# Optimization experiments

Measured on AMD Instinct MI355X. Metric: run time of the kernel, lower is better.

The kernel has to match this reference:

```python
import jax, jax.numpy as jnp
import numpy as np

VOCAB, EMB, HID, LABELS, NUM_LAYERS = 32000, 512, 1024, 64, 2
B, S = 32, 512


def setup_inputs() -> dict:
    key = jax.random.key(0)
    ks = jax.random.split(key, 12)
    s_e = 1.0 / np.sqrt(EMB)
    s_h = 1.0 / np.sqrt(HID)
    inp = {
        "tokens": jax.random.randint(ks[0], (B, S), 0, VOCAB),
        "emb": jax.random.normal(ks[1], (VOCAB, EMB), jnp.float32),
        # layer 0: input dim EMB
        "W_ih0": jax.random.uniform(ks[2], (HID, EMB), jnp.float32, -s_h, s_h),
        "W_hh0": jax.random.uniform(ks[3], (HID, HID), jnp.float32, -s_h, s_h),
        "b_ih0": jax.random.uniform(ks[4], (HID,), jnp.float32, -s_h, s_h),
        "b_hh0": jax.random.uniform(ks[5], (HID,), jnp.float32, -s_h, s_h),
        # layer 1: input dim HID
        "W_ih1": jax.random.uniform(ks[6], (HID, HID), jnp.float32, -s_h, s_h),
        "W_hh1": jax.random.uniform(ks[7], (HID, HID), jnp.float32, -s_h, s_h),
        "b_ih1": jax.random.uniform(ks[8], (HID,), jnp.float32, -s_h, s_h),
        "b_hh1": jax.random.uniform(ks[9], (HID,), jnp.float32, -s_h, s_h),
        "W_out": jax.random.uniform(ks[10], (LABELS, HID), jnp.float32, -s_h, s_h),
        "b_out": jax.random.uniform(ks[11], (LABELS,), jnp.float32, -s_h, s_h),
    }
    return inp


def _rnn_layer(x, W_ih, W_hh, b_ih, b_hh):
    # x: [B,S,in] -> h_t = tanh(W_ih x_t + b_ih + W_hh h_{t-1} + b_hh)
    # Precompute input projection for all timesteps (one big GEMM).
    xp = jnp.einsum('bsi,hi->bsh', x, W_ih) + (b_ih + b_hh)  # [B,S,H]
    h0 = jnp.zeros((x.shape[0], W_hh.shape[0]), x.dtype)

    def step(h, xt):
        h = jnp.tanh(xt + h @ W_hh.T)
        return h, h

    _, ys = jax.lax.scan(step, h0, jnp.swapaxes(xp, 0, 1))  # [S,B,H]
    return jnp.swapaxes(ys, 0, 1)  # [B,S,H]


def reference(tokens, emb, W_ih0, W_hh0, b_ih0, b_hh0,
              W_ih1, W_hh1, b_ih1, b_hh1, W_out, b_out):
    x = emb[tokens]  # [B,S,EMB]
    h = _rnn_layer(x, W_ih0, W_hh0, b_ih0, b_hh0)
    h = _rnn_layer(h, W_ih1, W_hh1, b_ih1, b_hh1)
    return jnp.einsum('bsh,lh->bsl', h, W_out) + b_out  # [B,S,LABELS]
```

## Files before the change

### kernel.cpp

```cpp
#include <hip/hip_runtime.h>
#include <math.h>

#define B_    32
#define S_    512
#define EMB_  512
#define HID_  1024
#define LAB_  64
#define M_    (B_ * S_)

#define SLOT_U64   2048
#define LS_STRIDE  (8 * SLOT_U64)
#define EX_TOTAL   (2 * 4 * LS_STRIDE)
#define EPBIT      0x40000000u
#define NANPAT64   0x7FC000007FC00000ULL
#define ONEPAT64   0x3F8000003F800000ULL
#define PAYMASK    0xBFFFFFFFu

typedef unsigned int u32x4 __attribute__((ext_vector_type(4)));

__device__ __forceinline__ void astore64(unsigned long long* p, unsigned long long v) {
    __hip_atomic_store(p, v, __ATOMIC_RELAXED, __HIP_MEMORY_SCOPE_AGENT);
}
__device__ __forceinline__ void apoll2(const unsigned long long* q0,
                                       const unsigned long long* q1,
                                       u32x4& w0, u32x4& w1) {
    asm volatile(
        "global_load_dwordx4 %0, %2, off sc1\n\t"
        "global_load_dwordx4 %1, %3, off sc1\n\t"
        "s_waitcnt vmcnt(0)"
        : "=&v"(w0), "=&v"(w1)
        : "v"(q0), "v"(q1)
        : "memory");
}
__device__ __forceinline__ bool epok4(u32x4 v, unsigned eb) {
    return ((((v[0] ^ eb) | (v[1] ^ eb)) | ((v[2] ^ eb) | (v[3] ^ eb)))
            & EPBIT) == 0;
}
__device__ __forceinline__ float fold16(float* v, int kg) {
#pragma unroll
    for (int st = 0; st < 4; ++st) {
        const int m  = 1 << st;
        const int nh = 8 >> st;
        const bool hi = (kg & m) != 0;
#pragma unroll
        for (int j = 0; j < 8; ++j) {
            if (j < nh) {
                const float a0 = v[2*j], a1 = v[2*j+1];
                const float got = __shfl_xor(hi ? a0 : a1, m, 64);
                v[j] = (hi ? a1 : a0) + got;
            }
        }
    }
    float r = v[0];
    r += __shfl_xor(r, 16, 64);
    r += __shfl_xor(r, 32, 64);
    return r;
}

__global__ __launch_bounds__(256) void gemm_bias(
    const float* __restrict__ A, const int* __restrict__ tokens,
    const float* __restrict__ W, const float* __restrict__ bias,
    const float* __restrict__ bias2, float* __restrict__ C,
    int M, int K, int N)
{
    __shared__ float As[128][17];
    __shared__ float Ws[64][17];

    const int tid = threadIdx.x;
    const int tx  = tid & 15;
    const int ty  = tid >> 4;
    const int n0  = blockIdx.x * 64;
    const int m0  = blockIdx.y * 128;

    const int lr  = tid >> 2;
    const int lk  = (tid & 3) << 2;

    const int ar0 = tokens ? tokens[m0 + lr]      : (m0 + lr);
    const int ar1 = tokens ? tokens[m0 + 64 + lr] : (m0 + 64 + lr);
    const float* __restrict__ arow0 = A + (size_t)ar0 * K;
    const float* __restrict__ arow1 = A + (size_t)ar1 * K;
    const float* __restrict__ wrow  = W + (size_t)(n0 + lr) * K;

    float bs[4];
#pragma unroll
    for (int j = 0; j < 4; ++j) {
        int n = n0 + tx * 4 + j;
        bs[j] = bias[n] + (bias2 ? bias2[n] : 0.0f);
    }

    float acc[8][4] = {};

    for (int k0 = 0; k0 < K; k0 += 16) {
        const float4 a0 = *(const float4*)(arow0 + k0 + lk);
        const float4 a1 = *(const float4*)(arow1 + k0 + lk);
        const float4 wv = *(const float4*)(wrow  + k0 + lk);
        __syncthreads();
        As[lr][lk + 0] = a0.x; As[lr][lk + 1] = a0.y;
        As[lr][lk + 2] = a0.z; As[lr][lk + 3] = a0.w;
        As[64 + lr][lk + 0] = a1.x; As[64 + lr][lk + 1] = a1.y;
        As[64 + lr][lk + 2] = a1.z; As[64 + lr][lk + 3] = a1.w;
        Ws[lr][lk + 0] = wv.x; Ws[lr][lk + 1] = wv.y;
        Ws[lr][lk + 2] = wv.z; Ws[lr][lk + 3] = wv.w;
        __syncthreads();

#pragma unroll
        for (int kk = 0; kk < 16; ++kk) {
            float b[4], a[8];
#pragma unroll
            for (int j = 0; j < 4; ++j) b[j] = Ws[tx * 4 + j][kk];
#pragma unroll
            for (int i = 0; i < 8; ++i) a[i] = As[ty * 8 + i][kk];
#pragma unroll
            for (int i = 0; i < 8; ++i)
#pragma unroll
                for (int j = 0; j < 4; ++j)
                    acc[i][j] += a[i] * b[j];
        }
    }

#pragma unroll
    for (int i = 0; i < 8; ++i) {
        const int m = m0 + ty * 8 + i;
        float4 v;
        v.x = acc[i][0] + bs[0];
        v.y = acc[i][1] + bs[1];
        v.z = acc[i][2] + bs[2];
        v.w = acc[i][3] + bs[3];
        *(float4*)(C + (size_t)m * N + n0 + tx * 4) = v;
    }
}

__global__ __launch_bounds__(256) void fill_poison(unsigned long long* p, int n)
{
    const int i = blockIdx.x * 256 + threadIdx.x;
    if (i < n) {
        const int ls = i / LS_STRIDE;
        p[i] = (ls == 4) ? ONEPAT64 : NANPAT64;
    }
}

__global__ __launch_bounds__(512, 2) void rnn_fused(
    const float* __restrict__ Whh0, const float* __restrict__ Whh1,
    const float* __restrict__ Wih1, const float* __restrict__ b_ih1,
    const float* __restrict__ b_hh1, float* __restrict__ xb,
    unsigned long long* __restrict__ ex)
{
    extern __shared__ float smem[];
    float2* hb = (float2*)smem;

    const int wg  = blockIdx.x;
    const int g   = wg & 7;
    const int s   = wg >> 3;
    const int tid = threadIdx.x;
    const int j8  = tid >> 6;
    const int kg  = tid & 63;
    const int b0  = g * 4;

    float w0[4][16], wx[4][16], wh[4][16];
    {
        const size_t base = (size_t)(s * 32 + j8 * 4) * HID_ + kg;
#pragma unroll
        for (int i = 0; i < 4; ++i)
#pragma unroll
            for (int q = 0; q < 16; ++q) {
                const size_t o = base + (size_t)i * HID_ + (size_t)q * 64;
                w0[i][q] = Whh0[o];
                wx[i][q] = Wih1[o];
                wh[i][q] = Whh1[o];
            }
    }

    const int i4 = (kg >> 2) & 3;
    const int bb = kg & 3;
    const int ok = s * 32 + j8 * 4 + i4;
    float bsum = 0.f;
    if (kg < 16) bsum = b_ih1[ok] + b_hh1[ok];

    float* px0 = xb + ((size_t)(b0 + bb) * S_) * HID_ + ok;
    float* px1 = px0;

    unsigned long long* const exg = ex + (size_t)g * SLOT_U64;
    const int c0 = 2 * tid, c1 = 1024 + 2 * tid;

    for (int r = 0; r <= S_; ++r) {
        float xpv = 0.f;
        if (kg < 16 && r < S_) xpv = *px0;
        px0 += HID_;

        const int cur = r & 1;
        float2* s0 = hb + (size_t)cur * 2048;
        float2* s1 = hb + (size_t)(2 + cur) * 2048;

        const int sl = (r - 1) & 3;
        const unsigned eb = ((((unsigned)(r - 1)) >> 2) & 1u) << 30;

        if (r == 0) {
#pragma unroll
            for (int k = 0; k < 4; ++k)
                s0[tid + 512 * k] = make_float2(0.f, 0.f);
        } else {
            const unsigned long long* pl = exg + (size_t)sl * LS_STRIDE;
            unsigned pend = 3u;
            u32x4 w0v, w1v;
            do {
                apoll2(pl + c0, pl + c1, w0v, w1v);
                if ((pend & 1u) && epok4(w0v, eb)) {
                    s0[tid]        = make_float2(
                        __uint_as_float(w0v[0] & PAYMASK),
                        __uint_as_float(w0v[1] & PAYMASK));
                    s0[1024 + tid] = make_float2(
                        __uint_as_float(w0v[2] & PAYMASK),
                        __uint_as_float(w0v[3] & PAYMASK));
                    pend &= ~1u;
                }
                if ((pend & 2u) && epok4(w1v, eb)) {
                    s0[512 + tid]  = make_float2(
                        __uint_as_float(w1v[0] & PAYMASK),
                        __uint_as_float(w1v[1] & PAYMASK));
                    s0[1536 + tid] = make_float2(
                        __uint_as_float(w1v[2] & PAYMASK),
                        __uint_as_float(w1v[3] & PAYMASK));
                    pend &= ~2u;
                }
            } while (pend);
        }
        __syncthreads();

        {
            float v[16] = {};
#pragma unroll
            for (int q = 0; q < 16; ++q) {
                const float2 a0 = s0[q * 64 + kg];
                const float2 a1 = s0[1024 + q * 64 + kg];
#pragma unroll
                for (int i = 0; i < 4; ++i) {
                    const float fa = w0[i][q];
                    v[i*4+0] += fa * a0.x; v[i*4+1] += fa * a0.y;
                    v[i*4+2] += fa * a1.x; v[i*4+3] += fa * a1.y;
                }
            }
            const float r0 = fold16(v, kg);
            if (r < S_) {
                float h0 = 0.f;
                if (kg < 16) h0 = tanhf(xpv + r0);
                const float h0p = __shfl_xor(h0, 1, 64);
                if (kg < 16 && (bb & 1) == 0) {
                    const unsigned pe = (((unsigned)r >> 2) & 1u) << 30;
                    const unsigned long long u =
                        ((unsigned long long)(__float_as_uint(h0p) | pe) << 32) |
                        (unsigned long long)(__float_as_uint(h0) | pe);
                    astore64(exg + (size_t)(r & 3) * LS_STRIDE
                                 + 2 * ok + (bb >> 1), u);
                }
            }
        }

        if (r == 1) {
#pragma unroll
            for (int k = 0; k < 4; ++k)
                s1[tid + 512 * k] = make_float2(0.f, 0.f);
        } else if (r >= 2) {
            const unsigned long long* pl = exg + (size_t)(4 + sl) * LS_STRIDE;
            unsigned pend = 3u;
            u32x4 w0v, w1v;
            do {
                apoll2(pl + c0, pl + c1, w0v, w1v);
                if ((pend & 1u) && epok4(w0v, eb)) {
                    s1[tid]        = make_float2(
                        __uint_as_float(w0v[0] & PAYMASK),
                        __uint_as_float(w0v[1] & PAYMASK));
                    s1[1024 + tid] = make_float2(
                        __uint_as_float(w0v[2] & PAYMASK),
                        __uint_as_float(w0v[3] & PAYMASK));
                    pend &= ~1u;
                }
                if ((pend & 2u) && epok4(w1v, eb)) {
                    s1[512 + tid]  = make_float2(
                        __uint_as_float(w1v[0] & PAYMASK),
                        __uint_as_float(w1v[1] & PAYMASK));
                    s1[1536 + tid] = make_float2(
                        __uint_as_float(w1v[2] & PAYMASK),
                        __uint_as_float(w1v[3] & PAYMASK));
                    pend &= ~2u;
                }
            } while (pend);
        }
        __syncthreads();

        if (r >= 1) {
            float v[16] = {};
#pragma unroll
            for (int q = 0; q < 16; ++q) {
                const float2 a0 = s0[q * 64 + kg];
                const float2 a1 = s0[1024 + q * 64 + kg];
                const float2 c0f = s1[q * 64 + kg];
                const float2 c1f = s1[1024 + q * 64 + kg];
#pragma unroll
                for (int i = 0; i < 4; ++i) {
                    const float fb = wx[i][q];
                    v[i*4+0] += fb * a0.x; v[i*4+1] += fb * a0.y;
                    v[i*4+2] += fb * a1.x; v[i*4+3] += fb * a1.y;
                    const float fc = wh[i][q];
                    v[i*4+0] += fc * c0f.x; v[i*4+1] += fc * c0f.y;
                    v[i*4+2] += fc * c1f.x; v[i*4+3] += fc * c1f.y;
                }
            }
            const float r1 = fold16(v, kg);
            float h1 = 0.f;
            if (kg < 16) h1 = tanhf(r1 + bsum);
            const float h1p = __shfl_xor(h1, 1, 64);
            if (kg < 16) *px1 = h1;
            if (kg < 16 && (bb & 1) == 0) {
                const unsigned pe = (((unsigned)r >> 2) & 1u) << 30;
                const unsigned long long u =
                    ((unsigned long long)(__float_as_uint(h1p) | pe) << 32) |
                    (unsigned long long)(__float_as_uint(h1) | pe);
                astore64(exg + (size_t)(4 + (r & 3)) * LS_STRIDE
                             + 2 * ok + (bb >> 1), u);
            }
            px1 += HID_;
        }
    }
}

extern "C" void kernel_launch(void* const* d_in, const int* in_sizes, int n_in,
                              void* d_out, int out_size, void* d_ws, size_t ws_size,
                              hipStream_t stream)
{
    const int*   tokens = (const int*)  d_in[0];
    const float* emb    = (const float*)d_in[1];
    const float* W_ih0  = (const float*)d_in[2];
    const float* W_hh0  = (const float*)d_in[3];
    const float* b_ih0  = (const float*)d_in[4];
    const float* b_hh0  = (const float*)d_in[5];
    const float* W_ih1  = (const float*)d_in[6];
    const float* W_hh1  = (const float*)d_in[7];
    const float* b_ih1  = (const float*)d_in[8];
    const float* b_hh1  = (const float*)d_in[9];
    const float* W_out  = (const float*)d_in[10];
    const float* b_out  = (const float*)d_in[11];
    float* out = (float*)d_out;

    float* buf = (float*)d_ws;
    unsigned long long* ex = (unsigned long long*)d_out;

    const size_t scan_lds = 98304;
    hipFuncSetAttribute((const void*)rnn_fused,
                        hipFuncAttributeMaxDynamicSharedMemorySize, (int)scan_lds);

    gemm_bias<<<dim3(HID_ / 64, M_ / 128), 256, 0, stream>>>(
        emb, tokens, W_ih0, b_ih0, b_hh0, buf, M_, EMB_, HID_);

    fill_poison<<<EX_TOTAL / 256, 256, 0, stream>>>(ex, EX_TOTAL);

    rnn_fused<<<256, 512, scan_lds, stream>>>(
        W_hh0, W_hh1, W_ih1, b_ih1, b_hh1, buf, ex);

    gemm_bias<<<dim3(LAB_ / 64, M_ / 128), 256, 0, stream>>>(
        buf, nullptr, W_out, b_out, nullptr, out, M_, HID_, LAB_);
}
```

Measured before the change: 3.258 ms.

## Skew layer-1 recurrence by two steps and merge both polls into one barrier

Layer 1 now runs two steps behind layer 0 and reads layer-0 state from a triple-buffered shared slot. Both exchange polls (layer-0 h at r-1 and layer-1 h at r-3) therefore happen in a single combined wait loop with one __syncthreads per step instead of two. This removes a serialized global poll and barrier from each timestep's critical path, letting the cross-workgroup latencies of the two layers overlap. It costs one extra loop iteration, more LDS buffers, and more complex epoch and slot indexing, which could cause hangs or wrong results if any index is off.

```diff
diff --git a/kernel.cpp b/kernel.cpp
--- a/kernel.cpp
+++ b/kernel.cpp
@@ -13,7 +13,6 @@
 #define EX_TOTAL   (2 * 4 * LS_STRIDE)
 #define EPBIT      0x40000000u
 #define NANPAT64   0x7FC000007FC00000ULL
-#define ONEPAT64   0x3F8000003F800000ULL
 #define PAYMASK    0xBFFFFFFFu
 
 typedef unsigned int u32x4 __attribute__((ext_vector_type(4)));
@@ -133,10 +132,7 @@
 __global__ __launch_bounds__(256) void fill_poison(unsigned long long* p, int n)
 {
     const int i = blockIdx.x * 256 + threadIdx.x;
-    if (i < n) {
-        const int ls = i / LS_STRIDE;
-        p[i] = (ls == 4) ? ONEPAT64 : NANPAT64;
-    }
+    if (i < n) p[i] = NANPAT64;
 }
 
 __global__ __launch_bounds__(512, 2) void rnn_fused(
@@ -182,56 +178,90 @@
     unsigned long long* const exg = ex + (size_t)g * SLOT_U64;
     const int c0 = 2 * tid, c1 = 1024 + 2 * tid;
 
-    for (int r = 0; r <= S_; ++r) {
+    for (int r = 0; r <= S_ + 1; ++r) {
         float xpv = 0.f;
         if (kg < 16 && r < S_) xpv = *px0;
         px0 += HID_;
 
-        const int cur = r & 1;
-        float2* s0 = hb + (size_t)cur * 2048;
-        float2* s1 = hb + (size_t)(2 + cur) * 2048;
-
-        const int sl = (r - 1) & 3;
-        const unsigned eb = ((((unsigned)(r - 1)) >> 2) & 1u) << 30;
+        float2* sA = hb + (size_t)(r % 3) * 2048;
+        float2* sP = hb + (size_t)((r + 2) % 3) * 2048;
+        float2* s1 = hb + (size_t)(3 + (r & 1)) * 2048;
 
         if (r == 0) {
 #pragma unroll
             for (int k = 0; k < 4; ++k)
-                s0[tid + 512 * k] = make_float2(0.f, 0.f);
-        } else {
-            const unsigned long long* pl = exg + (size_t)sl * LS_STRIDE;
-            unsigned pend = 3u;
-            u32x4 w0v, w1v;
-            do {
-                apoll2(pl + c0, pl + c1, w0v, w1v);
-                if ((pend & 1u) && epok4(w0v, eb)) {
-                    s0[tid]        = make_float2(
-                        __uint_as_float(w0v[0] & PAYMASK),
-                        __uint_as_float(w0v[1] & PAYMASK));
-                    s0[1024 + tid] = make_float2(
-                        __uint_as_float(w0v[2] & PAYMASK),
-                        __uint_as_float(w0v[3] & PAYMASK));
-                    pend &= ~1u;
-                }
-                if ((pend & 2u) && epok4(w1v, eb)) {
-                    s0[512 + tid]  = make_float2(
-                        __uint_as_float(w1v[0] & PAYMASK),
-                        __uint_as_float(w1v[1] & PAYMASK));
-                    s0[1536 + tid] = make_float2(
-                        __uint_as_float(w1v[2] & PAYMASK),
-                        __uint_as_float(w1v[3] & PAYMASK));
-                    pend &= ~2u;
-                }
-            } while (pend);
+                sA[tid + 512 * k] = make_float2(0.f, 0.f);
+        }
+        if (r == 2) {
+#pragma unroll
+            for (int k = 0; k < 4; ++k)
+                s1[tid + 512 * k] = make_float2(0.f, 0.f);
+        }
+        {
+            unsigned pend = ((r >= 1 && r <= S_) ? 3u : 0u)
+                          | ((r >= 3) ? 0xCu : 0u);
+            if (pend) {
+                const unsigned long long* pl0 =
+                    exg + (size_t)((r - 1) & 3) * LS_STRIDE;
+                const unsigned long long* pl1 =
+                    exg + (size_t)(4 + ((r - 3) & 3)) * LS_STRIDE;
+                const unsigned eb0 = ((((unsigned)(r - 1)) >> 2) & 1u) << 30;
+                const unsigned eb1 = ((((unsigned)(r - 3)) >> 2) & 1u) << 30;
+                u32x4 a0, a1, d0, d1;
+                do {
+                    if (pend & 3u) {
+                        apoll2(pl0 + c0, pl0 + c1, a0, a1);
+                        if ((pend & 1u) && epok4(a0, eb0)) {
+                            sA[tid]        = make_float2(
+                                __uint_as_float(a0[0] & PAYMASK),
+                                __uint_as_float(a0[1] & PAYMASK));
+                            sA[1024 + tid] = make_float2(
+                                __uint_as_float(a0[2] & PAYMASK),
+                                __uint_as_float(a0[3] & PAYMASK));
+                            pend &= ~1u;
+                        }
+                        if ((pend & 2u) && epok4(a1, eb0)) {
+                            sA[512 + tid]  = make_float2(
+                                __uint_as_float(a1[0] & PAYMASK),
+                                __uint_as_float(a1[1] & PAYMASK));
+                            sA[1536 + tid] = make_float2(
+                                __uint_as_float(a1[2] & PAYMASK),
+                                __uint_as_float(a1[3] & PAYMASK));
+                            pend &= ~2u;
+                        }
+                    }
+                    if (pend & 0xCu) {
+                        apoll2(pl1 + c0, pl1 + c1, d0, d1);
+                        if ((pend & 4u) && epok4(d0, eb1)) {
+                            s1[tid]        = make_float2(
+                                __uint_as_float(d0[0] & PAYMASK),
+                                __uint_as_float(d0[1] & PAYMASK));
+                            s1[1024 + tid] = make_float2(
+                                __uint_as_float(d0[2] & PAYMASK),
+                                __uint_as_float(d0[3] & PAYMASK));
+                            pend &= ~4u;
+                        }
+                        if ((pend & 8u) && epok4(d1, eb1)) {
+                            s1[512 + tid]  = make_float2(
+                                __uint_as_float(d1[0] & PAYMASK),
+                                __uint_as_float(d1[1] & PAYMASK));
+                            s1[1536 + tid] = make_float2(
+                                __uint_as_float(d1[2] & PAYMASK),
+                                __uint_as_float(d1[3] & PAYMASK));
+                            pend &= ~8u;
+                        }
+                    }
+                } while (pend);
+            }
         }
         __syncthreads();
 
-        {
+        if (r < S_) {
             float v[16] = {};
 #pragma unroll
             for (int q = 0; q < 16; ++q) {
-                const float2 a0 = s0[q * 64 + kg];
-                const float2 a1 = s0[1024 + q * 64 + kg];
+                const float2 a0 = sA[q * 64 + kg];
+                const float2 a1 = sA[1024 + q * 64 + kg];
 #pragma unroll
                 for (int i = 0; i < 4; ++i) {
                     const float fa = w0[i][q];
@@ -240,59 +270,25 @@
                 }
             }
             const float r0 = fold16(v, kg);
-            if (r < S_) {
-                float h0 = 0.f;
-                if (kg < 16) h0 = tanhf(xpv + r0);
-                const float h0p = __shfl_xor(h0, 1, 64);
-                if (kg < 16 && (bb & 1) == 0) {
-                    const unsigned pe = (((unsigned)r >> 2) & 1u) << 30;
-                    const unsigned long long u =
-                        ((unsigned long long)(__float_as_uint(h0p) | pe) << 32) |
-                        (unsigned long long)(__float_as_uint(h0) | pe);
-                    astore64(exg + (size_t)(r & 3) * LS_STRIDE
-                                 + 2 * ok + (bb >> 1), u);
-                }
-            }
-        }
-
-        if (r == 1) {
-#pragma unroll
-            for (int k = 0; k < 4; ++k)
-                s1[tid + 512 * k] = make_float2(0.f, 0.f);
-        } else if (r >= 2) {
-            const unsigned long long* pl = exg + (size_t)(4 + sl) * LS_STRIDE;
-            unsigned pend = 3u;
-            u32x4 w0v, w1v;
-            do {
-                apoll2(pl + c0, pl + c1, w0v, w1v);
-                if ((pend & 1u) && epok4(w0v, eb)) {
-                    s1[tid]        = make_float2(
-                        __uint_as_float(w0v[0] & PAYMASK),
-                        __uint_as_float(w0v[1] & PAYMASK));
-                    s1[1024 + tid] = make_float2(
-                        __uint_as_float(w0v[2] & PAYMASK),
-                        __uint_as_float(w0v[3] & PAYMASK));
-                    pend &= ~1u;
-                }
-                if ((pend & 2u) && epok4(w1v, eb)) {
-                    s1[512 + tid]  = make_float2(
-                        __uint_as_float(w1v[0] & PAYMASK),
-                        __uint_as_float(w1v[1] & PAYMASK));
-                    s1[1536 + tid] = make_float2(
-                        __uint_as_float(w1v[2] & PAYMASK),
-                        __uint_as_float(w1v[3] & PAYMASK));
-                    pend &= ~2u;
-                }
-            } while (pend);
-        }
-        __syncthreads();
-
-        if (r >= 1) {
+            float h0 = 0.f;
+            if (kg < 16) h0 = tanhf(xpv + r0);
+            const float h0p = __shfl_xor(h0, 1, 64);
+            if (kg < 16 && (bb & 1) == 0) {
+                const unsigned pe = (((unsigned)r >> 2) & 1u) << 30;
+                const unsigned long long u =
+                    ((unsigned long long)(__float_as_uint(h0p) | pe) << 32) |
+                    (unsigned long long)(__float_as_uint(h0) | pe);
+                astore64(exg + (size_t)(r & 3) * LS_STRIDE
+                             + 2 * ok + (bb >> 1), u);
+            }
+        }
+
+        if (r >= 2) {
             float v[16] = {};
 #pragma unroll
             for (int q = 0; q < 16; ++q) {
-                const float2 a0 = s0[q * 64 + kg];
-                const float2 a1 = s0[1024 + q * 64 + kg];
+                const float2 a0 = sP[q * 64 + kg];
+                const float2 a1 = sP[1024 + q * 64 + kg];
                 const float2 c0f = s1[q * 64 + kg];
                 const float2 c1f = s1[1024 + q * 64 + kg];
 #pragma unroll
@@ -311,11 +307,11 @@
             const float h1p = __shfl_xor(h1, 1, 64);
             if (kg < 16) *px1 = h1;
             if (kg < 16 && (bb & 1) == 0) {
-                const unsigned pe = (((unsigned)r >> 2) & 1u) << 30;
+                const unsigned pe = (((unsigned)(r - 2) >> 2) & 1u) << 30;
                 const unsigned long long u =
                     ((unsigned long long)(__float_as_uint(h1p) | pe) << 32) |
                     (unsigned long long)(__float_as_uint(h1) | pe);
-                astore64(exg + (size_t)(4 + (r & 3)) * LS_STRIDE
+                astore64(exg + (size_t)(4 + ((r - 2) & 3)) * LS_STRIDE
                              + 2 * ok + (bb >> 1), u);
             }
             px1 += HID_;
```

Measured after the change: 3.132 ms. 3.9% less time.
